# Kernel optimization log

Measured on AMD Instinct MI355X. Metric: run time of the kernel, lower is better.

Reference implementation:

```python
import jax, jax.numpy as jnp
import numpy as np
from jax import lax


def _box_conv3d(x, win):
    k = jnp.ones((1, 1, win, win, win), x.dtype) / float(win ** 3)
    pad = win // 2
    return lax.conv_general_dilated(
        x, k,
        window_strides=(1, 1, 1),
        padding=[(pad, pad)] * 3,
        dimension_numbers=('NCDHW', 'OIDHW', 'NCDHW'),
    )


def setup_inputs() -> dict:
    key = jax.random.key(0)
    k1, k2 = jax.random.split(key)
    shape = (1, 1, 160, 192, 224)
    pred = jax.random.uniform(k1, shape, dtype=jnp.float32)
    target = jax.random.uniform(k2, shape, dtype=jnp.float32)
    return {'pred': pred, 'target': target, 'window_size': 9}


def reference(pred, target, window_size):
    Ii = target
    Ji = pred
    win = window_size
    mu1 = _box_conv3d(Ii, win)
    mu2 = _box_conv3d(Ji, win)
    mu1_sq = mu1 * mu1
    mu2_sq = mu2 * mu2
    mu1_mu2 = mu1 * mu2
    sigma1_sq = _box_conv3d(Ii * Ii, win) - mu1_sq
    sigma2_sq = _box_conv3d(Ji * Ji, win) - mu2_sq
    sigma12 = _box_conv3d(Ii * Ji, win) - mu1_mu2
    eps = jnp.finfo(sigma12.dtype).eps
    cc = sigma12 * sigma12 / jnp.maximum(sigma1_sq * sigma2_sq, eps)
    return -jnp.mean(cc)
```

## Files before the change

kernel.cpp:

```cpp
#include <hip/hip_runtime.h>
#include <hip/hip_fp16.h>

#define D_  160
#define H_  192
#define W_  224
#define HW_ (H_ * W_)
#define HW2_ (HW_ / 2)
#define N_  (D_ * H_ * W_)
#define INV729 (1.0f / 729.0f)
#define HSEG 16
#define NSEG (H_ / HSEG)
#define NROW (HSEG + 9)
#define UPD  (NSEG * 2)


__device__ __forceinline__ unsigned pack2(float a, float b) {
    const __half2 h = __floats2half2_rn(a, b);
    return *(const unsigned*)&h;
}

__global__ __launch_bounds__(64) void k_passWH(const float* __restrict__ pred,
                                               const float* __restrict__ targ,
                                               uint4* __restrict__ outA,
                                               unsigned* __restrict__ outB,
                                               double* __restrict__ acc) {
    __shared__ __attribute__((aligned(16))) float2 lds[2][2][128];
    if (blockIdx.x == 0 && threadIdx.x == 0) *acc = 0.0;

    const int lane = threadIdx.x;
    const int unit = blockIdx.x;
    const int dp   = unit / UPD;
    const int rem  = unit % UPD;
    const int half = rem & 1;
    const int h0   = (rem >> 1) * HSEG;
    const long dbaseA = (long)dp * HW_;
    const long dbaseB = (long)(dp + 80) * HW_;
    const int wbase = half * 112;

    const int  sj   = (lane < 30) ? lane : lane - 30;
    const int  w0c  = wbase - 4 + 4 * sj;
    const bool cokG = (lane < 60) && (w0c >= 0) && (w0c + 3 < W_);
    const int  wsc  = w0c < 0 ? 0 : (w0c > W_ - 4 ? W_ - 4 : w0c);
    const long sdb  = (lane < 30) ? dbaseA : dbaseB;
    const int  sstr = (lane < 30) ? 0 : 1;
    const float* gI = targ + sdb + wsc;
    const float* gJ = pred + sdb + wsc;

    unsigned q[2][5][9];
    #pragma unroll
    for (int s = 0; s < 2; ++s)
        #pragma unroll
        for (int c = 0; c < 5; ++c)
            #pragma unroll
            for (int k = 0; k < 9; ++k) q[s][c][k] = 0u;
    float S0[2][5] = {{0,0,0,0,0},{0,0,0,0,0}};
    float S1[2][5] = {{0,0,0,0,0},{0,0,0,0,0}};

    float4 pI[4], pJ[4];
    auto fetch = [&](int r, float4& fi, float4& fj) {
        if (r >= NROW) { fi = make_float4(0.f,0.f,0.f,0.f); fj = fi; return; }
        const int hh = h0 - 5 + r;
        const int hc = hh < 0 ? 0 : (hh >= H_ ? H_ - 1 : hh);
        float4 a = *(const float4*)(gI + (long)hc * W_);
        float4 b = *(const float4*)(gJ + (long)hc * W_);
        if (!(cokG && hh >= 0 && hh < H_)) {
            a = make_float4(0.f, 0.f, 0.f, 0.f); b = a;
        }
        fi = a; fj = b;
    };
    auto wr = [&](int row, int slot) {
        float2* dst = &lds[sstr][row & 1][4 * sj];
        *(float4*)(dst)     = make_float4(pI[slot].x, pJ[slot].x, pI[slot].y, pJ[slot].y);
        *(float4*)(dst + 2) = make_float4(pI[slot].z, pJ[slot].z, pI[slot].w, pJ[slot].w);
    };

    if (lane < 60) {
        fetch(0, pI[0], pJ[0]);
        fetch(1, pI[1], pJ[1]);
        fetch(2, pI[2], pJ[2]);
        fetch(3, pI[3], pJ[3]);
        wr(0, 0);
        fetch(4, pI[0], pJ[0]);
    }

    #pragma unroll
    for (int p = 0; p < NROW; ++p) {
        if (lane < 56) {
            const int ph = p % 9;
            #pragma unroll
            for (int s = 0; s < 2; ++s) {
                float x[10], y[10];
                #pragma unroll
                for (int m = 0; m < 5; ++m) {
                    const float4 v = *(const float4*)&lds[s][p & 1][2 * lane + 2 * m];
                    x[2*m] = v.x; y[2*m] = v.y; x[2*m+1] = v.z; y[2*m+1] = v.w;
                }
                float sI = 0.f, sJ = 0.f, sII = 0.f, sJJ = 0.f, sIJ = 0.f;
                #pragma unroll
                for (int kk = 0; kk < 9; ++kk) {
                    sI  += x[kk];          sJ  += y[kk];
                    sII = fmaf(x[kk], x[kk], sII);
                    sJJ = fmaf(y[kk], y[kk], sJJ);
                    sIJ = fmaf(x[kk], y[kk], sIJ);
                }
                float w0s[5], w1s[5];
                w0s[0] = sI;  w1s[0] = sI  + x[9] - x[0];
                w0s[1] = sJ;  w1s[1] = sJ  + y[9] - y[0];
                w0s[2] = sII; w1s[2] = sII + x[9]*x[9] - x[0]*x[0];
                w0s[3] = sJJ; w1s[3] = sJJ + y[9]*y[9] - y[0]*y[0];
                w0s[4] = sIJ; w1s[4] = sIJ + x[9]*y[9] - x[0]*y[0];

                #pragma unroll
                for (int c = 0; c < 5; ++c) {
                    const unsigned nq = pack2(w0s[c], w1s[c]);
                    const float2 nf = __half22float2(*(const __half2*)&nq);
                    const float2 of = __half22float2(*(const __half2*)&q[s][c][ph]);
                    S0[s][c] += nf.x - of.x;
                    S1[s][c] += nf.y - of.y;
                    q[s][c][ph] = nq;
                }
                if (p >= 9) {
                    const long db = s ? dbaseB : dbaseA;
                    const long rb = db + (long)(h0 + p - 9) * W_;
                    uint4 oA;
                    oA.x = pack2(S0[s][0], S0[s][1]); oA.y = pack2(S0[s][2], S0[s][3]);
                    oA.z = pack2(S1[s][0], S1[s][1]); oA.w = pack2(S1[s][2], S1[s][3]);
                    outA[rb / 2 + half * 56 + lane] = oA;
                    outB[rb / 2 + half * 56 + lane] = pack2(S0[s][4], S1[s][4]);
                }
            }
        }

        if (lane < 60) {
            wr(p + 1, (p + 1) & 3);
            fetch(p + 5, pI[(p + 1) & 3], pJ[(p + 1) & 3]);
        }
    }
}

__global__ __launch_bounds__(256) void k_passD(const uint4* __restrict__ bufA,
                                               const unsigned* __restrict__ bufB,
                                               double* __restrict__ acc) {
    const int DSEG = D_ / 8;
    const int p2 = blockIdx.x * blockDim.x + threadIdx.x;
    const int d0 = blockIdx.y * DSEG;

    float2 q[5][9], S[5];
    #pragma unroll
    for (int c = 0; c < 5; ++c) S[c] = make_float2(0.f, 0.f);

    #pragma unroll
    for (int k = 0; k < 9; ++k) {
        const int dd = d0 - 5 + k;
        uint4 va = make_uint4(0u, 0u, 0u, 0u);
        unsigned vb = 0u;
        if (dd >= 0) {
            va = bufA[(long)dd * HW2_ + p2];
            vb = bufB[(long)dd * HW2_ + p2];
        }
        const float2 a01 = __half22float2(*(const __half2*)&va.x);
        const float2 a23 = __half22float2(*(const __half2*)&va.y);
        const float2 b01 = __half22float2(*(const __half2*)&va.z);
        const float2 b23 = __half22float2(*(const __half2*)&va.w);
        const float2 c44 = __half22float2(*(const __half2*)&vb);
        q[0][k] = make_float2(a01.x, b01.x); S[0].x += a01.x; S[0].y += b01.x;
        q[1][k] = make_float2(a01.y, b01.y); S[1].x += a01.y; S[1].y += b01.y;
        q[2][k] = make_float2(a23.x, b23.x); S[2].x += a23.x; S[2].y += b23.x;
        q[3][k] = make_float2(a23.y, b23.y); S[3].x += a23.y; S[3].y += b23.y;
        q[4][k] = make_float2(c44.x, c44.y); S[4].x += c44.x; S[4].y += c44.y;
    }

    float myacc = 0.f;
    #pragma unroll
    for (int j = 0; j < DSEG; ++j) {
        const int dd = d0 + 4 + j;
        uint4 va = make_uint4(0u, 0u, 0u, 0u);
        unsigned vb = 0u;
        if (dd < D_) {
            va = bufA[(long)dd * HW2_ + p2];
            vb = bufB[(long)dd * HW2_ + p2];
        }
        const float2 a01 = __half22float2(*(const __half2*)&va.x);
        const float2 a23 = __half22float2(*(const __half2*)&va.y);
        const float2 b01 = __half22float2(*(const __half2*)&va.z);
        const float2 b23 = __half22float2(*(const __half2*)&va.w);
        const float2 c44 = __half22float2(*(const __half2*)&vb);
        const float2 nv[5] = {
            make_float2(a01.x, b01.x), make_float2(a01.y, b01.y),
            make_float2(a23.x, b23.x), make_float2(a23.y, b23.y),
            make_float2(c44.x, c44.y)
        };
        const int ph = j % 9;
        #pragma unroll
        for (int c = 0; c < 5; ++c) {
            S[c].x += nv[c].x - q[c][ph].x;
            S[c].y += nv[c].y - q[c][ph].y;
            q[c][ph] = nv[c];
        }
        #pragma unroll
        for (int e = 0; e < 2; ++e) {
            const float mu1 = (e ? S[0].y : S[0].x) * INV729;
            const float mu2 = (e ? S[1].y : S[1].x) * INV729;
            const float s1  = (e ? S[2].y : S[2].x) * INV729 - mu1 * mu1;
            const float s2  = (e ? S[3].y : S[3].x) * INV729 - mu2 * mu2;
            const float s12 = (e ? S[4].y : S[4].x) * INV729 - mu1 * mu2;
            const float den = fmaxf(s1 * s2, 1.1920929e-7f);
            myacc += (s12 * s12) / den;
        }
    }

    __shared__ float red[256];
    red[threadIdx.x] = myacc;
    __syncthreads();
    #pragma unroll
    for (int s = 128; s > 0; s >>= 1) {
        if (threadIdx.x < s) red[threadIdx.x] += red[threadIdx.x + s];
        __syncthreads();
    }
    if (threadIdx.x == 0) atomicAdd(acc, (double)red[0]);
}

__global__ void k_fin(const double* __restrict__ acc, float* __restrict__ out) {
    out[0] = (float)(-(*acc) / (double)N_);
}

extern "C" void kernel_launch(void* const* d_in, const int* in_sizes, int n_in,
                              void* d_out, int out_size, void* d_ws, size_t ws_size,
                              hipStream_t stream) {
    const float* pred = (const float*)d_in[0];
    const float* targ = (const float*)d_in[1];

    uint4*    bufA = (uint4*)d_ws;
    unsigned* bufB = (unsigned*)((char*)d_ws + (size_t)(N_ / 2) * 16);
    double*   acc  = (double*)((char*)d_ws + (size_t)(N_ / 2) * 16 + (size_t)(N_ / 2) * 4);
    float*    out  = (float*)d_out;

    k_passWH<<<80 * UPD, 64, 0, stream>>>(pred, targ, bufA, bufB, acc);
    dim3 g3(HW2_ / 256, 8);
    k_passD<<<g3, 256, 0, stream>>>(bufA, bufB, acc);
    k_fin<<<1, 1, 0, stream>>>(acc, out);
}
```

Before: 55.81 us.

## Replace fully unrolled row loop with rolled loop of four-row steps and shifting ring

The fully unrolled 25-row loop in the WH pass becomes a rolled loop of 7 iterations, each handling 4 rows unrolled. The 9-deep ring buffer is now indexed with compile-time constants and shifted by 4 at the end of each iteration. The aim is to cut instruction-cache footprint and code size while keeping ring indexing static in registers. In exchange it adds register moves for the shift and computes 28 rows instead of 25, with extra fetches past NROW masked to zero.

```diff
diff --git a/kernel.cpp b/kernel.cpp
--- a/kernel.cpp
+++ b/kernel.cpp
@@ -58,18 +58,17 @@
 
     float4 pI[4], pJ[4];
     auto fetch = [&](int r, float4& fi, float4& fj) {
-        if (r >= NROW) { fi = make_float4(0.f,0.f,0.f,0.f); fj = fi; return; }
         const int hh = h0 - 5 + r;
         const int hc = hh < 0 ? 0 : (hh >= H_ ? H_ - 1 : hh);
         float4 a = *(const float4*)(gI + (long)hc * W_);
         float4 b = *(const float4*)(gJ + (long)hc * W_);
-        if (!(cokG && hh >= 0 && hh < H_)) {
+        if (!(cokG && r < NROW && hh >= 0 && hh < H_)) {
             a = make_float4(0.f, 0.f, 0.f, 0.f); b = a;
         }
         fi = a; fj = b;
     };
-    auto wr = [&](int row, int slot) {
-        float2* dst = &lds[sstr][row & 1][4 * sj];
+    auto wr = [&](int buf, int slot) {
+        float2* dst = &lds[sstr][buf][4 * sj];
         *(float4*)(dst)     = make_float4(pI[slot].x, pJ[slot].x, pI[slot].y, pJ[slot].y);
         *(float4*)(dst + 2) = make_float4(pI[slot].z, pJ[slot].z, pI[slot].w, pJ[slot].w);
     };
@@ -83,58 +82,72 @@
         fetch(4, pI[0], pJ[0]);
     }
 
-    #pragma unroll
-    for (int p = 0; p < NROW; ++p) {
-        if (lane < 56) {
-            const int ph = p % 9;
-            #pragma unroll
-            for (int s = 0; s < 2; ++s) {
-                float x[10], y[10];
+    #pragma unroll 1
+    for (int it = 0; it < 7; ++it) {
+        unsigned nw[2][5][4];
+        #pragma unroll
+        for (int j = 0; j < 4; ++j) {
+            const int p = 4 * it + j;
+
+            if (lane < 56) {
                 #pragma unroll
-                for (int m = 0; m < 5; ++m) {
-                    const float4 v = *(const float4*)&lds[s][p & 1][2 * lane + 2 * m];
-                    x[2*m] = v.x; y[2*m] = v.y; x[2*m+1] = v.z; y[2*m+1] = v.w;
-                }
-                float sI = 0.f, sJ = 0.f, sII = 0.f, sJJ = 0.f, sIJ = 0.f;
-                #pragma unroll
-                for (int kk = 0; kk < 9; ++kk) {
-                    sI  += x[kk];          sJ  += y[kk];
-                    sII = fmaf(x[kk], x[kk], sII);
-                    sJJ = fmaf(y[kk], y[kk], sJJ);
-                    sIJ = fmaf(x[kk], y[kk], sIJ);
-                }
-                float w0s[5], w1s[5];
-                w0s[0] = sI;  w1s[0] = sI  + x[9] - x[0];
-                w0s[1] = sJ;  w1s[1] = sJ  + y[9] - y[0];
-                w0s[2] = sII; w1s[2] = sII + x[9]*x[9] - x[0]*x[0];
-                w0s[3] = sJJ; w1s[3] = sJJ + y[9]*y[9] - y[0]*y[0];
-                w0s[4] = sIJ; w1s[4] = sIJ + x[9]*y[9] - x[0]*y[0];
-
-                #pragma unroll
-                for (int c = 0; c < 5; ++c) {
-                    const unsigned nq = pack2(w0s[c], w1s[c]);
-                    const float2 nf = __half22float2(*(const __half2*)&nq);
-                    const float2 of = __half22float2(*(const __half2*)&q[s][c][ph]);
-                    S0[s][c] += nf.x - of.x;
-                    S1[s][c] += nf.y - of.y;
-                    q[s][c][ph] = nq;
-                }
-                if (p >= 9) {
-                    const long db = s ? dbaseB : dbaseA;
-                    const long rb = db + (long)(h0 + p - 9) * W_;
-                    uint4 oA;
-                    oA.x = pack2(S0[s][0], S0[s][1]); oA.y = pack2(S0[s][2], S0[s][3]);
-                    oA.z = pack2(S1[s][0], S1[s][1]); oA.w = pack2(S1[s][2], S1[s][3]);
-                    outA[rb / 2 + half * 56 + lane] = oA;
-                    outB[rb / 2 + half * 56 + lane] = pack2(S0[s][4], S1[s][4]);
+                for (int s = 0; s < 2; ++s) {
+                    float x[10], y[10];
+                    #pragma unroll
+                    for (int m = 0; m < 5; ++m) {
+                        const float4 v = *(const float4*)&lds[s][j & 1][2 * lane + 2 * m];
+                        x[2*m] = v.x; y[2*m] = v.y; x[2*m+1] = v.z; y[2*m+1] = v.w;
+                    }
+                    float sI = 0.f, sJ = 0.f, sII = 0.f, sJJ = 0.f, sIJ = 0.f;
+                    #pragma unroll
+                    for (int kk = 0; kk < 9; ++kk) {
+                        sI  += x[kk];          sJ  += y[kk];
+                        sII = fmaf(x[kk], x[kk], sII);
+                        sJJ = fmaf(y[kk], y[kk], sJJ);
+                        sIJ = fmaf(x[kk], y[kk], sIJ);
+                    }
+                    float w0s[5], w1s[5];
+                    w0s[0] = sI;  w1s[0] = sI  + x[9] - x[0];
+                    w0s[1] = sJ;  w1s[1] = sJ  + y[9] - y[0];
+                    w0s[2] = sII; w1s[2] = sII + x[9]*x[9] - x[0]*x[0];
+                    w0s[3] = sJJ; w1s[3] = sJJ + y[9]*y[9] - y[0]*y[0];
+                    w0s[4] = sIJ; w1s[4] = sIJ + x[9]*y[9] - x[0]*y[0];
+
+                    #pragma unroll
+                    for (int c = 0; c < 5; ++c) {
+                        const unsigned nq = pack2(w0s[c], w1s[c]);
+                        const float2 nf = __half22float2(*(const __half2*)&nq);
+                        const float2 of = __half22float2(*(const __half2*)&q[s][c][j]);
+                        S0[s][c] += nf.x - of.x;
+                        S1[s][c] += nf.y - of.y;
+                        nw[s][c][j] = nq;
+                    }
+                    if (p >= 9 && p <= 24 && lane < 56) {
+                        const long db = s ? dbaseB : dbaseA;
+                        const long rb = db + (long)(h0 + p - 9) * W_;
+                        uint4 oA;
+                        oA.x = pack2(S0[s][0], S0[s][1]); oA.y = pack2(S0[s][2], S0[s][3]);
+                        oA.z = pack2(S1[s][0], S1[s][1]); oA.w = pack2(S1[s][2], S1[s][3]);
+                        outA[rb / 2 + half * 56 + lane] = oA;
+                        outB[rb / 2 + half * 56 + lane] = pack2(S0[s][4], S1[s][4]);
+                    }
                 }
             }
-        }
-
-        if (lane < 60) {
-            wr(p + 1, (p + 1) & 3);
-            fetch(p + 5, pI[(p + 1) & 3], pJ[(p + 1) & 3]);
-        }
+
+            if (lane < 60) {
+                wr((j + 1) & 1, (j + 1) & 3);
+                fetch(p + 5, pI[(j + 1) & 3], pJ[(j + 1) & 3]);
+            }
+        }
+        #pragma unroll
+        for (int s = 0; s < 2; ++s)
+            #pragma unroll
+            for (int c = 0; c < 5; ++c) {
+                #pragma unroll
+                for (int k = 0; k < 5; ++k) q[s][c][k] = q[s][c][k + 4];
+                #pragma unroll
+                for (int j = 0; j < 4; ++j) q[s][c][5 + j] = nw[s][c][j];
+            }
     }
 }
 
```

New measurement: 62.54 us. +12.0%, slower.
